# Kernel optimization log

Measured on AMD Instinct MI355X. Metric: run time of the kernel, lower is better.

Reference implementation:

```python
import jax, jax.numpy as jnp
import numpy as np

D_MODEL = 1024
N_HEADS = 16
D_HEAD = D_MODEL // N_HEADS
EPS = 1e-5


def setup_inputs() -> dict:
    key = jax.random.key(0)
    ks = jax.random.split(key, 7)
    B, T = 4, 2048
    s = 1.0 / np.sqrt(D_MODEL)
    return {
        "x": jax.random.normal(ks[0], (B, T, D_MODEL), dtype=jnp.float32),
        "ln_g": jnp.ones((D_MODEL,), jnp.float32),
        "ln_b": jnp.zeros((D_MODEL,), jnp.float32),
        "W_qkv": jax.random.normal(ks[1], (D_MODEL, 3 * D_MODEL), jnp.float32) * s,
        "b_qkv": jnp.zeros((3 * D_MODEL,), jnp.float32),
        "W_gate": jax.random.normal(ks[2], (D_MODEL, D_MODEL), jnp.float32) * s,
        "b_gate": jnp.zeros((D_MODEL,), jnp.float32),
        "W_proj": jax.random.normal(ks[3], (D_MODEL, D_MODEL), jnp.float32) * s,
        "b_proj": jnp.zeros((D_MODEL,), jnp.float32),
    }


def _forward(x, ln_g, ln_b, W_qkv, b_qkv, W_gate, b_gate, W_proj, b_proj):
    B, T, D = x.shape
    H, d = N_HEADS, D_HEAD
    # LayerNorm (eps=1e-5, biased variance as in torch)
    mu = jnp.mean(x, axis=-1, keepdims=True)
    var = jnp.mean((x - mu) ** 2, axis=-1, keepdims=True)
    x_norm = (x - mu) * jax.lax.rsqrt(var + EPS) * ln_g + ln_b
    qkv = x_norm @ W_qkv + b_qkv
    q, k, v = jnp.split(qkv, 3, axis=-1)  # each [B,T,D]
    # concept gate uses raw x
    gate = jax.nn.sigmoid(x @ W_gate + b_gate)
    gate = gate / (jnp.mean(gate, axis=-1, keepdims=True) + EPS)
    q = (q * gate).reshape(B, T, H, d)
    k = (k * gate).reshape(B, T, H, d)
    v = v.reshape(B, T, H, d)
    # ReLU^2 feature map in fp32
    q = jax.nn.relu(q.astype(jnp.float32)) ** 2 + EPS
    k = jax.nn.relu(k.astype(jnp.float32)) ** 2 + EPS
    v = v.astype(jnp.float32)
    # causal linear attention via kv recurrence (scan over T, T-major)
    qT = jnp.transpose(q, (1, 0, 2, 3))  # [T,B,H,d]
    kT = jnp.transpose(k, (1, 0, 2, 3))
    vT = jnp.transpose(v, (1, 0, 2, 3))

    def step(carry, inp):
        kv_s, k_s = carry  # [B,H,d,d], [B,H,d]
        q_t, k_t, v_t = inp  # [B,H,d]
        kv_s = kv_s + k_t[..., :, None] * v_t[..., None, :]
        k_s = k_s + k_t
        num = jnp.einsum('bhd,bhdm->bhm', q_t, kv_s)
        den = jnp.einsum('bhd,bhd->bh', q_t, k_s)[..., None] + EPS
        return (kv_s, k_s), num / den

    init = (jnp.zeros((B, H, d, d), jnp.float32), jnp.zeros((B, H, d), jnp.float32))
    _, outT = jax.lax.scan(step, init, (qT, kT, vT))  # [T,B,H,d]
    out = jnp.transpose(outT, (1, 0, 2, 3)).astype(x.dtype).reshape(B, T, D)
    return out @ W_proj + b_proj


def reference(x, ln_g, ln_b, W_qkv, b_qkv, W_gate, b_gate, W_proj, b_proj):
    return _forward(x, ln_g, ln_b, W_qkv, b_qkv, W_gate, b_gate, W_proj, b_proj)
```

## Files before the change

kernel.cpp:

```cpp
#include <hip/hip_runtime.h>
#include <math.h>

#define TOK 8192
#define DM 1024
#define EPSF 1e-5f

typedef __attribute__((ext_vector_type(8))) short short8;
typedef __attribute__((ext_vector_type(4))) float f32x4;

static __device__ __forceinline__ ushort f2bf(float f) {
  unsigned u = __float_as_uint(f);
  unsigned r = (u + 0x7fffu + ((u >> 16) & 1u)) >> 16;
  return (ushort)r;
}
static __device__ __forceinline__ float bf2f(ushort u) {
  return __uint_as_float((unsigned)u << 16);
}

static __device__ __forceinline__ void gload_lds16(const ushort* g, ushort* l) {
  __builtin_amdgcn_global_load_lds((const __attribute__((address_space(1))) void*)g,
                                   (__attribute__((address_space(3))) void*)l, 16, 0, 0);
}

static __device__ __forceinline__ int cswz(int row) {
  return (((row & 7) ^ ((row >> 3) & 7)) << 3);
}

__global__ __launch_bounds__(256) void prep_k(
    const float* __restrict__ x, const float* __restrict__ g,
    const float* __restrict__ b, ushort* __restrict__ x_b,
    ushort* __restrict__ xn_b,
    const float* __restrict__ Wg, const float* __restrict__ Wq,
    const float* __restrict__ Wp, ushort* __restrict__ Wtg,
    ushort* __restrict__ Wtq, ushort* __restrict__ Wtp) {
  __shared__ ushort tile[32][33];
  __shared__ float red[8];
  if (blockIdx.x < 8192) {
    int row = blockIdx.x;
    const float4* xr = (const float4*)(x + (size_t)row * DM);
    float4 v = xr[threadIdx.x];
    ushort4 xb4;
    xb4.x = f2bf(v.x); xb4.y = f2bf(v.y); xb4.z = f2bf(v.z); xb4.w = f2bf(v.w);
    ((ushort4*)(x_b + (size_t)row * DM))[threadIdx.x] = xb4;
    float s = v.x + v.y + v.z + v.w;
#pragma unroll
    for (int o = 32; o > 0; o >>= 1) s += __shfl_down(s, o, 64);
    int lane = threadIdx.x & 63, w = threadIdx.x >> 6;
    if (lane == 0) red[w] = s;
    __syncthreads();
    float mu = (red[0] + red[1] + red[2] + red[3]) * (1.0f / DM);
    float dx = v.x - mu, dy = v.y - mu, dz = v.z - mu, dw = v.w - mu;
    float ss = dx * dx + dy * dy + dz * dz + dw * dw;
#pragma unroll
    for (int o = 32; o > 0; o >>= 1) ss += __shfl_down(ss, o, 64);
    if (lane == 0) red[4 + w] = ss;
    __syncthreads();
    float var = (red[4] + red[5] + red[6] + red[7]) * (1.0f / DM);
    float rstd = rsqrtf(var + EPSF);
    float4 gg = ((const float4*)g)[threadIdx.x];
    float4 bb = ((const float4*)b)[threadIdx.x];
    ushort4 o4;
    o4.x = f2bf(dx * rstd * gg.x + bb.x);
    o4.y = f2bf(dy * rstd * gg.y + bb.y);
    o4.z = f2bf(dz * rstd * gg.z + bb.z);
    o4.w = f2bf(dw * rstd * gg.w + bb.w);
    ((ushort4*)(xn_b + (size_t)row * DM))[threadIdx.x] = o4;
  } else {
    int bid = blockIdx.x - 8192;
    const float* W; ushort* Wt; int N; int local;
    if (bid < 1024)      { W = Wg; Wt = Wtg; N = 1024; local = bid; }
    else if (bid < 4096) { W = Wq; Wt = Wtq; N = 3072; local = bid - 1024; }
    else                 { W = Wp; Wt = Wtp; N = 1024; local = bid - 4096; }
    int ntiles = N >> 5;
    int n0 = (local % ntiles) * 32, k0 = (local / ntiles) * 32;
    int tx = threadIdx.x & 31, ty = threadIdx.x >> 5;
#pragma unroll
    for (int i = 0; i < 4; i++) {
      int k = ty + i * 8;
      tile[k][tx] = f2bf(W[(size_t)(k0 + k) * N + n0 + tx]);
    }
    __syncthreads();
#pragma unroll
    for (int i = 0; i < 4; i++) {
      int n = ty + i * 8;
      Wt[(size_t)(n0 + n) * 1024 + k0 + tx] = tile[tx][n];
    }
  }
}

#define BM 128
#define BN 128
#define BK 64

static __device__ __forceinline__ void stage_tile128(
    const ushort* __restrict__ A, const ushort* __restrict__ Bt,
    int m0, int n0, int k0, int K, ushort* As, ushort* Bs, int w, int lane) {
#pragma unroll
  for (int j = 0; j < 4; j++) {
    int lu = (w * 4 + j) * 64 + lane;
    int r = lu >> 3;
    int kb = (lu & 7) ^ (r & 7);
    gload_lds16(A + (size_t)(m0 + r) * K + k0 + kb * 8, As + (w * 4 + j) * 512);
    gload_lds16(Bt + (size_t)(n0 + r) * K + k0 + kb * 8, Bs + (w * 4 + j) * 512);
  }
}

static __device__ __forceinline__ void compute_tile128(
    const ushort* as, const ushort* bs, int wr, int wc, int lane, f32x4 acc[4][4]) {
#pragma unroll
  for (int ks = 0; ks < 2; ks++) {
    short8 af[4], bfr[4];
    int kq = ks * 4 + (lane >> 4);
#pragma unroll
    for (int f = 0; f < 4; f++) {
      int ra = wr * 64 + f * 16 + (lane & 15);
      af[f] = *(const short8*)&as[(ra * 8 + (kq ^ (ra & 7))) * 8];
      int rb = wc * 64 + f * 16 + (lane & 15);
      bfr[f] = *(const short8*)&bs[(rb * 8 + (kq ^ (rb & 7))) * 8];
    }
#pragma unroll
    for (int i = 0; i < 4; i++)
#pragma unroll
      for (int j2 = 0; j2 < 4; j2++)
        acc[i][j2] = __builtin_amdgcn_mfma_f32_16x16x32_bf16(af[i], bfr[j2], acc[i][j2], 0, 0, 0);
  }
}

#define GEMM_LOOP128(A_, B_, m0_, n0_, K_)                                       \
  f32x4 acc[4][4] = {};                                                          \
  stage_tile128(A_, B_, m0_, n0_, 0, K_, sh, sh + 16384, w, lane);               \
  int nt = (K_) / BK;                                                            \
  for (int t = 0; t < nt; t++) {                                                 \
    __syncthreads();                                                             \
    if (t + 1 < nt)                                                              \
      stage_tile128(A_, B_, m0_, n0_, (t + 1) * BK, K_,                          \
                    sh + ((t + 1) & 1) * 8192, sh + 16384 + ((t + 1) & 1) * 8192,\
                    w, lane);                                                    \
    compute_tile128(sh + (t & 1) * 8192, sh + 16384 + (t & 1) * 8192,            \
                    wr, wc, lane, acc);                                          \
  }                                                                              \
  __syncthreads();

__global__ __launch_bounds__(256) void gemm_bf16_k(
    const ushort* __restrict__ A, const ushort* __restrict__ Bt,
    const float* __restrict__ bias, float* __restrict__ Cf, int ldc, int K) {
  __shared__ __align__(16) ushort sh[32768];
  int tid = threadIdx.x, lane = tid & 63, w = tid >> 6;
  int m0 = blockIdx.y * BM, n0 = blockIdx.x * BN;
  int wr = w >> 1, wc = w & 1;
  GEMM_LOOP128(A, Bt, m0, n0, K)
#pragma unroll
  for (int i = 0; i < 4; i++) {
#pragma unroll
    for (int j2 = 0; j2 < 4; j2++) {
      int col = n0 + wc * 64 + j2 * 16 + (lane & 15);
      float bv = bias[col];
#pragma unroll
      for (int r = 0; r < 4; r++) {
        int row = m0 + wr * 64 + i * 16 + (lane >> 4) * 4 + r;
        Cf[(size_t)row * ldc + col] = acc[i][j2][r] + bv;
      }
    }
  }
}

__global__ __launch_bounds__(256) void gemm_gate_k(
    const ushort* __restrict__ A, const ushort* __restrict__ Bt,
    const float* __restrict__ bias, ushort* __restrict__ Cb, int ldc, int K,
    float* __restrict__ gpart) {
  __shared__ __align__(16) ushort sh[32768];
  int tid = threadIdx.x, lane = tid & 63, w = tid >> 6;
  int m0 = blockIdx.y * BM, n0 = blockIdx.x * BN;
  int wr = w >> 1, wc = w & 1;
  GEMM_LOOP128(A, Bt, m0, n0, K)
  int lr = lane & 15, lg = lane >> 4;
  float* rs2 = (float*)sh;
#pragma unroll
  for (int i = 0; i < 4; i++) {
#pragma unroll
    for (int r = 0; r < 4; r++) {
      float rsum = 0.0f;
      int row = m0 + wr * 64 + i * 16 + lg * 4 + r;
#pragma unroll
      for (int j2 = 0; j2 < 4; j2++) {
        int col = n0 + wc * 64 + j2 * 16 + lr;
        float v = 1.0f / (1.0f + __expf(-(acc[i][j2][r] + bias[col])));
        rsum += v;
        Cb[(size_t)row * ldc + col] = f2bf(v);
      }
#pragma unroll
      for (int o = 1; o < 16; o <<= 1) rsum += __shfl_xor(rsum, o, 64);
      if (lr == 0) rs2[wc * 128 + wr * 64 + i * 16 + lg * 4 + r] = rsum;
    }
  }
  __syncthreads();
  if (tid < 128)
    gpart[(size_t)(m0 + tid) * 8 + blockIdx.x] = rs2[tid] + rs2[128 + tid];
}

__global__ __launch_bounds__(256) void gemm_qkv_k(
    const ushort* __restrict__ A, const ushort* __restrict__ Bt,
    const float* __restrict__ bias, const ushort* __restrict__ gate_b,
    const float* __restrict__ gpart,
    ushort* __restrict__ qb, ushort* __restrict__ kb,
    ushort* __restrict__ kt, ushort* __restrict__ vt, int K) {
  __shared__ __align__(16) ushort sh[32768];
  __shared__ float ginvs[128];
  int tid = threadIdx.x, lane = tid & 63, w = tid >> 6;
  int m0 = blockIdx.y * BM, n0 = blockIdx.x * BN;
  int wr = w >> 1, wc = w & 1;
  GEMM_LOOP128(A, Bt, m0, n0, K)
  int region = n0 >> 10;
  int n0b = n0 & 1023;
  int h0 = n0b >> 6;
  if (region < 2) {
    if (tid < 128) {
      const float4* gp = (const float4*)&gpart[(size_t)(m0 + tid) * 8];
      float4 s0 = gp[0], s1 = gp[1];
      float s = s0.x + s0.y + s0.z + s0.w + s1.x + s1.y + s1.z + s1.w;
      ginvs[tid] = 1.0f / (s * (1.0f / DM) + EPSF);
    }
#pragma unroll
    for (int it = 0; it < 8; it++) {
      int e = it * 256 + tid;
      int row = e >> 4, ch = e & 15;
      *(short8*)&sh[row * 132 + ch * 8] =
          *(const short8*)&gate_b[(size_t)(m0 + row) * DM + n0b + ch * 8];
    }
    __syncthreads();
#pragma unroll
    for (int i = 0; i < 4; i++) {
#pragma unroll
      for (int j2 = 0; j2 < 4; j2++) {
        int cl = wc * 64 + j2 * 16 + (lane & 15);
        float bv = bias[n0 + cl];
        int rl0 = wr * 64 + i * 16 + (lane >> 4) * 4;
#pragma unroll
        for (int r = 0; r < 4; r++) {
          float gv = bf2f(sh[(rl0 + r) * 132 + cl]) * ginvs[rl0 + r];
          float v = (acc[i][j2][r] + bv) * gv;
          v = fmaxf(v, 0.0f);
          acc[i][j2][r] = v * v + EPSF;
        }
      }
    }
    __syncthreads();
  } else {
#pragma unroll
    for (int i = 0; i < 4; i++)
#pragma unroll
      for (int j2 = 0; j2 < 4; j2++) {
        int cl = wc * 64 + j2 * 16 + (lane & 15);
        float bv = bias[n0 + cl];
#pragma unroll
        for (int r = 0; r < 4; r++) acc[i][j2][r] += bv;
      }
  }
#pragma unroll
  for (int i = 0; i < 4; i++) {
#pragma unroll
    for (int j2 = 0; j2 < 4; j2++) {
      int cl = wc * 64 + j2 * 16 + (lane & 15);
      int rl0 = wr * 64 + i * 16 + (lane >> 4) * 4;
#pragma unroll
      for (int r = 0; r < 4; r++) {
        int row = rl0 + r;
        sh[row * 128 + (cl ^ cswz(row))] = f2bf(acc[i][j2][r]);
      }
    }
  }
  __syncthreads();
  if (region < 2) {
    ushort* dstRM = (region == 0) ? qb : kb;
#pragma unroll
    for (int it = 0; it < 8; it++) {
      int e = it * 256 + tid;
      int row = e >> 4, ch = e & 15;
      short8 val = *(const short8*)&sh[row * 128 + ((ch * 8) ^ cswz(row))];
      int tglob = m0 + row;
      size_t bh2 = (size_t)(tglob >> 11) * 16 + h0 + (ch >> 3);
      *(short8*)&dstRM[(bh2 * 2048 + (tglob & 2047)) * 64 + (ch & 7) * 8] = val;
    }
  }
  if (region >= 1) {
    ushort* dstT = (region == 1) ? kt : vt;
#pragma unroll
    for (int it = 0; it < 8; it++) {
      int e = it * 256 + tid;
      int tch = e & 15, dkrow = e >> 4;
      short8 val;
#pragma unroll
      for (int j = 0; j < 8; j++) {
        int row = tch * 8 + j;
        val[j] = (short)sh[row * 128 + (dkrow ^ cswz(row))];
      }
      int tglob0 = m0 + tch * 8;
      size_t bh2 = (size_t)(tglob0 >> 11) * 16 + h0 + (dkrow >> 6);
      *(short8*)&dstT[(bh2 * 64 + (dkrow & 63)) * 2048 + (tglob0 & 2047)] = val;
    }
  }
}

__global__ __launch_bounds__(256) void chunkpfx_k(const ushort* __restrict__ kt,
                                                  const ushort* __restrict__ vt,
                                                  ushort* __restrict__ KVb,
                                                  float* __restrict__ ksum) {
  int bid = blockIdx.x;
  int bh = (bid & 7) | ((bid >> 5) << 3);
  int dvs = (bid >> 3) & 3;
  int tid = threadIdx.x, l = tid & 63, w = tid >> 6;
  int lg = l >> 4;
  const ushort* vT = vt + ((size_t)bh * 64 + dvs * 16 + (l & 15)) * 2048;
  const ushort* kT = kt + ((size_t)bh * 64 + w * 16 + (l & 15)) * 2048;
  f32x4 run = {0.f, 0.f, 0.f, 0.f};
  float runks = 0.0f;
  short8 a0 = *(const short8*)&vT[lg * 8];
  short8 a1 = *(const short8*)&vT[32 + lg * 8];
  short8 b0 = *(const short8*)&kT[lg * 8];
  short8 b1 = *(const short8*)&kT[32 + lg * 8];
  for (int c = 0; c < 32; c++) {
    ushort* dst = KVb + ((size_t)bh * 32 + c) * 4096 +
                  (size_t)(dvs * 16 + lg * 4) * 64 + w * 16 + (l & 15);
    dst[0] = f2bf(run[0]); dst[64] = f2bf(run[1]);
    dst[128] = f2bf(run[2]); dst[192] = f2bf(run[3]);
    if (dvs == 0) {
      float s = 0.f;
#pragma unroll
      for (int j = 0; j < 8; j++) s += bf2f((ushort)b0[j]) + bf2f((ushort)b1[j]);
      s += __shfl_xor(s, 16, 64);
      s += __shfl_xor(s, 32, 64);
      if (l < 16) ksum[((size_t)bh * 32 + c) * 64 + w * 16 + l] = runks;
      runks += s;
    }
    int cn = (c + 1) & 31;
    short8 na0 = *(const short8*)&vT[cn * 64 + lg * 8];
    short8 na1 = *(const short8*)&vT[cn * 64 + 32 + lg * 8];
    short8 nb0 = *(const short8*)&kT[cn * 64 + lg * 8];
    short8 nb1 = *(const short8*)&kT[cn * 64 + 32 + lg * 8];
    run = __builtin_amdgcn_mfma_f32_16x16x32_bf16(a0, b0, run, 0, 0, 0);
    run = __builtin_amdgcn_mfma_f32_16x16x32_bf16(a1, b1, run, 0, 0, 0);
    a0 = na0; a1 = na1; b0 = nb0; b1 = nb1;
  }
}

__global__ __launch_bounds__(256) void attn_k(
    const ushort* __restrict__ qb, const ushort* __restrict__ kb,
    const ushort* __restrict__ vt, const ushort* __restrict__ KVb,
    const float* __restrict__ ks, ushort* __restrict__ attnout) {
  int c = blockIdx.x, bh = blockIdx.y;
  int b = bh >> 4, h = bh & 15;
  const ushort* qB = qb + ((size_t)bh * 2048 + (size_t)c * 64) * 64;
  const ushort* kB = kb + ((size_t)bh * 2048 + (size_t)c * 64) * 64;
  const ushort* vT = vt + (size_t)bh * 64 * 2048 + (size_t)c * 64;
  const ushort* kvB = KVb + ((size_t)bh * 32 + c) * 4096;
  const float* ksP = ks + ((size_t)bh * 32 + c) * 64;
  __shared__ __align__(16) char SL[64 * 128];
  __shared__ float denp[4][64];
  __shared__ float den2p[4][64];
  __shared__ float invden[64];
  int tid = threadIdx.x, l = tid & 63, w = tid >> 6;
  int lr = l & 15, lg = l >> 4;
  {
    short8 q0 = *(const short8*)&qB[(size_t)l * 64 + w * 16];
    short8 q1 = *(const short8*)&qB[(size_t)l * 64 + w * 16 + 8];
    float d2 = 0.0f;
#pragma unroll
    for (int j = 0; j < 8; j++) {
      d2 += bf2f((ushort)q0[j]) * ksP[w * 16 + j];
      d2 += bf2f((ushort)q1[j]) * ksP[w * 16 + 8 + j];
    }
    den2p[w][l] = d2;
  }
#pragma unroll
  for (int n = 0; n < 4; n++) {
    f32x4 sa = {0.f, 0.f, 0.f, 0.f};
#pragma unroll
    for (int g = 0; g < 2; g++) {
      short8 a = *(const short8*)&kB[(size_t)(w * 16 + lr) * 64 + g * 32 + lg * 8];
      short8 bq = *(const short8*)&qB[(size_t)(n * 16 + lr) * 64 + g * 32 + lg * 8];
      sa = __builtin_amdgcn_mfma_f32_16x16x32_bf16(a, bq, sa, 0, 0, 0);
    }
    int t = n * 16 + lr;
    int s0 = w * 16 + lg * 4;
    float dsum = 0.0f;
    ushort sb[4];
#pragma unroll
    for (int r = 0; r < 4; r++) {
      float v = (s0 + r <= t) ? sa[r] : 0.0f;
      dsum += v;
      sb[r] = f2bf(v);
    }
    dsum += __shfl_xor(dsum, 16, 64);
    dsum += __shfl_xor(dsum, 32, 64);
    if (l < 16) denp[w][n * 16 + l] = dsum;
    int u = (s0 >> 3) ^ (t & 7);
    uint2 p;
    p.x = sb[0] | ((unsigned)sb[1] << 16);
    p.y = sb[2] | ((unsigned)sb[3] << 16);
    *(uint2*)&SL[t * 128 + u * 16 + (s0 & 7) * 2] = p;
  }
  __syncthreads();
  if (tid < 64) {
    float den = denp[0][tid] + denp[1][tid] + denp[2][tid] + denp[3][tid] +
                den2p[0][tid] + den2p[1][tid] + den2p[2][tid] + den2p[3][tid] + EPSF;
    invden[tid] = 1.0f / den;
  }
  __syncthreads();
#pragma unroll
  for (int n = 0; n < 4; n++) {
    f32x4 oa = {0.f, 0.f, 0.f, 0.f};
#pragma unroll
    for (int g = 0; g < 2; g++) {
      short8 a = *(const short8*)&kvB[(size_t)(w * 16 + lr) * 64 + g * 32 + lg * 8];
      short8 bq = *(const short8*)&qB[(size_t)(n * 16 + lr) * 64 + g * 32 + lg * 8];
      oa = __builtin_amdgcn_mfma_f32_16x16x32_bf16(a, bq, oa, 0, 0, 0);
    }
    int t = n * 16 + lr;
#pragma unroll
    for (int g = 0; g < 2; g++) {
      short8 a = *(const short8*)&vT[(size_t)(w * 16 + lr) * 2048 + g * 32 + lg * 8];
      int u = (g * 4 + lg) ^ (t & 7);
      short8 bs = *(const short8*)&SL[t * 128 + u * 16];
      oa = __builtin_amdgcn_mfma_f32_16x16x32_bf16(a, bs, oa, 0, 0, 0);
    }
    float iv = invden[t];
    ushort ob[4];
#pragma unroll
    for (int r = 0; r < 4; r++) ob[r] = f2bf(oa[r] * iv);
    size_t tok = (size_t)b * 2048 + (size_t)c * 64 + t;
    uint2 p;
    p.x = ob[0] | ((unsigned)ob[1] << 16);
    p.y = ob[2] | ((unsigned)ob[3] << 16);
    *(uint2*)&attnout[tok * 1024 + h * 64 + w * 16 + lg * 4] = p;
  }
}

extern "C" void kernel_launch(void* const* d_in, const int* in_sizes, int n_in,
                              void* d_out, int out_size, void* d_ws, size_t ws_size,
                              hipStream_t stream) {
  const float* x      = (const float*)d_in[0];
  const float* ln_g   = (const float*)d_in[1];
  const float* ln_b   = (const float*)d_in[2];
  const float* W_qkv  = (const float*)d_in[3];
  const float* b_qkv  = (const float*)d_in[4];
  const float* W_gate = (const float*)d_in[5];
  const float* b_gate = (const float*)d_in[6];
  const float* W_proj = (const float*)d_in[7];
  const float* b_proj = (const float*)d_in[8];
  float* out = (float*)d_out;

  char* wsb = (char*)d_ws;
  const size_t TD = (size_t)TOK * DM;
  const size_t SLOT = TD * 2;
  ushort* x_b     = (ushort*)(wsb + 0 * SLOT);
  ushort* attnout = (ushort*)(wsb + 0 * SLOT);
  ushort* xn_b    = (ushort*)(wsb + 1 * SLOT);
  ushort* qb      = (ushort*)(wsb + 2 * SLOT);
  ushort* kb      = (ushort*)(wsb + 3 * SLOT);
  ushort* kt      = (ushort*)(wsb + 4 * SLOT);
  ushort* vt      = (ushort*)(wsb + 5 * SLOT);
  ushort* gate_b  = (ushort*)(wsb + 6 * SLOT);
  ushort* Wt_qkv  = (ushort*)(wsb + 8 * SLOT);
  ushort* Wt_gate = (ushort*)(wsb + 8 * SLOT + (size_t)8 * 1024 * 1024);
  ushort* KVb     = (ushort*)(wsb + 8 * SLOT);
  ushort* Wt_proj = (ushort*)(wsb + 9 * SLOT);
  float*  ksum    = (float*)(wsb + 9 * SLOT + (size_t)8 * 1024 * 1024);
  float*  gpart   = (float*)(wsb + 9 * SLOT + (size_t)12 * 1024 * 1024);

  prep_k<<<8192 + 5120, 256, 0, stream>>>(x, ln_g, ln_b, x_b, xn_b,
                                          W_gate, W_qkv, W_proj,
                                          Wt_gate, Wt_qkv, Wt_proj);
  gemm_gate_k<<<dim3(DM / BN, TOK / BM), 256, 0, stream>>>(x_b, Wt_gate, b_gate,
                                                           gate_b, DM, DM, gpart);
  gemm_qkv_k<<<dim3(3 * DM / BN, TOK / BM), 256, 0, stream>>>(xn_b, Wt_qkv, b_qkv, gate_b,
                                                              gpart, qb, kb, kt, vt, DM);
  chunkpfx_k<<<256, 256, 0, stream>>>(kt, vt, KVb, ksum);
  attn_k<<<dim3(32, 64), 256, 0, stream>>>(qb, kb, vt, KVb, ksum, attnout);
  gemm_bf16_k<<<dim3(DM / BN, TOK / BM), 256, 0, stream>>>(attnout, Wt_proj, b_proj, out,
                                                           DM, DM);
}
```

Baseline: 187.0 us.

## Fuse chunk prefix-state kernel into attention kernel with sequential chunk loop

Merges the chunk KV prefix-sum kernel and the per-chunk attention kernel into one kernel. Each block owns a (batch-head, 16-wide dv slice) and walks all 32 chunks in order, keeping the running KV state in registers and staging it through LDS instead of writing KVb and ksum to global memory. This removes a kernel launch and the global round trip for the chunk states. In exchange it drops from 2048 parallel blocks to 256 serial-over-chunks blocks, and the intra-chunk QK^T scores and denominator are recomputed by each of the four dv-slice blocks.

```diff
diff --git a/kernel.cpp b/kernel.cpp
--- a/kernel.cpp
+++ b/kernel.cpp
@@ -301,128 +301,110 @@
   }
 }
 
-__global__ __launch_bounds__(256) void chunkpfx_k(const ushort* __restrict__ kt,
-                                                  const ushort* __restrict__ vt,
-                                                  ushort* __restrict__ KVb,
-                                                  float* __restrict__ ksum) {
+__global__ __launch_bounds__(256) void attn_fused_k(
+    const ushort* __restrict__ qb, const ushort* __restrict__ kb,
+    const ushort* __restrict__ vt, const ushort* __restrict__ kt,
+    ushort* __restrict__ attnout) {
   int bid = blockIdx.x;
   int bh = (bid & 7) | ((bid >> 5) << 3);
   int dvs = (bid >> 3) & 3;
-  int tid = threadIdx.x, l = tid & 63, w = tid >> 6;
-  int lg = l >> 4;
-  const ushort* vT = vt + ((size_t)bh * 64 + dvs * 16 + (l & 15)) * 2048;
-  const ushort* kT = kt + ((size_t)bh * 64 + w * 16 + (l & 15)) * 2048;
-  f32x4 run = {0.f, 0.f, 0.f, 0.f};
-  float runks = 0.0f;
-  short8 a0 = *(const short8*)&vT[lg * 8];
-  short8 a1 = *(const short8*)&vT[32 + lg * 8];
-  short8 b0 = *(const short8*)&kT[lg * 8];
-  short8 b1 = *(const short8*)&kT[32 + lg * 8];
-  for (int c = 0; c < 32; c++) {
-    ushort* dst = KVb + ((size_t)bh * 32 + c) * 4096 +
-                  (size_t)(dvs * 16 + lg * 4) * 64 + w * 16 + (l & 15);
-    dst[0] = f2bf(run[0]); dst[64] = f2bf(run[1]);
-    dst[128] = f2bf(run[2]); dst[192] = f2bf(run[3]);
-    if (dvs == 0) {
-      float s = 0.f;
-#pragma unroll
-      for (int j = 0; j < 8; j++) s += bf2f((ushort)b0[j]) + bf2f((ushort)b1[j]);
-      s += __shfl_xor(s, 16, 64);
-      s += __shfl_xor(s, 32, 64);
-      if (l < 16) ksum[((size_t)bh * 32 + c) * 64 + w * 16 + l] = runks;
-      runks += s;
-    }
-    int cn = (c + 1) & 31;
-    short8 na0 = *(const short8*)&vT[cn * 64 + lg * 8];
-    short8 na1 = *(const short8*)&vT[cn * 64 + 32 + lg * 8];
-    short8 nb0 = *(const short8*)&kT[cn * 64 + lg * 8];
-    short8 nb1 = *(const short8*)&kT[cn * 64 + 32 + lg * 8];
-    run = __builtin_amdgcn_mfma_f32_16x16x32_bf16(a0, b0, run, 0, 0, 0);
-    run = __builtin_amdgcn_mfma_f32_16x16x32_bf16(a1, b1, run, 0, 0, 0);
-    a0 = na0; a1 = na1; b0 = nb0; b1 = nb1;
-  }
-}
-
-__global__ __launch_bounds__(256) void attn_k(
-    const ushort* __restrict__ qb, const ushort* __restrict__ kb,
-    const ushort* __restrict__ vt, const ushort* __restrict__ KVb,
-    const float* __restrict__ ks, ushort* __restrict__ attnout) {
-  int c = blockIdx.x, bh = blockIdx.y;
   int b = bh >> 4, h = bh & 15;
-  const ushort* qB = qb + ((size_t)bh * 2048 + (size_t)c * 64) * 64;
-  const ushort* kB = kb + ((size_t)bh * 2048 + (size_t)c * 64) * 64;
-  const ushort* vT = vt + (size_t)bh * 64 * 2048 + (size_t)c * 64;
-  const ushort* kvB = KVb + ((size_t)bh * 32 + c) * 4096;
-  const float* ksP = ks + ((size_t)bh * 32 + c) * 64;
+  const ushort* qB0 = qb + (size_t)bh * 2048 * 64;
+  const ushort* kB0 = kb + (size_t)bh * 2048 * 64;
+  const ushort* vT = vt + ((size_t)bh * 64 + dvs * 16) * 2048;
+  const ushort* kT = kt + (size_t)bh * 64 * 2048;
   __shared__ __align__(16) char SL[64 * 128];
+  __shared__ __align__(16) ushort KVL[16 * 64];
+  __shared__ float ksL[64];
   __shared__ float denp[4][64];
-  __shared__ float den2p[4][64];
   __shared__ float invden[64];
   int tid = threadIdx.x, l = tid & 63, w = tid >> 6;
   int lr = l & 15, lg = l >> 4;
-  {
-    short8 q0 = *(const short8*)&qB[(size_t)l * 64 + w * 16];
-    short8 q1 = *(const short8*)&qB[(size_t)l * 64 + w * 16 + 8];
-    float d2 = 0.0f;
-#pragma unroll
-    for (int j = 0; j < 8; j++) {
-      d2 += bf2f((ushort)q0[j]) * ksP[w * 16 + j];
-      d2 += bf2f((ushort)q1[j]) * ksP[w * 16 + 8 + j];
-    }
-    den2p[w][l] = d2;
-  }
-#pragma unroll
-  for (int n = 0; n < 4; n++) {
-    f32x4 sa = {0.f, 0.f, 0.f, 0.f};
+  f32x4 kvrun = {0.f, 0.f, 0.f, 0.f};
+  float runks = 0.0f;
+  for (int c = 0; c < 32; c++) {
+    const ushort* qB = qB0 + (size_t)c * 64 * 64;
+    const ushort* kB = kB0 + (size_t)c * 64 * 64;
+    short8 ka[2], ktf[2], vtf[2], bq[4][2];
 #pragma unroll
     for (int g = 0; g < 2; g++) {
-      short8 a = *(const short8*)&kB[(size_t)(w * 16 + lr) * 64 + g * 32 + lg * 8];
-      short8 bq = *(const short8*)&qB[(size_t)(n * 16 + lr) * 64 + g * 32 + lg * 8];
-      sa = __builtin_amdgcn_mfma_f32_16x16x32_bf16(a, bq, sa, 0, 0, 0);
-    }
-    int t = n * 16 + lr;
-    int s0 = w * 16 + lg * 4;
-    float dsum = 0.0f;
-    ushort sb[4];
+      ka[g]  = *(const short8*)&kB[(size_t)(w * 16 + lr) * 64 + g * 32 + lg * 8];
+      ktf[g] = *(const short8*)&kT[(size_t)(w * 16 + lr) * 2048 + c * 64 + g * 32 + lg * 8];
+      vtf[g] = *(const short8*)&vT[(size_t)lr * 2048 + c * 64 + g * 32 + lg * 8];
+#pragma unroll
+      for (int n = 0; n < 4; n++)
+        bq[n][g] = *(const short8*)&qB[(size_t)(n * 16 + lr) * 64 + g * 32 + lg * 8];
+    }
+#pragma unroll
+    for (int n = 0; n < 4; n++) {
+      f32x4 sa = {0.f, 0.f, 0.f, 0.f};
+      sa = __builtin_amdgcn_mfma_f32_16x16x32_bf16(ka[0], bq[n][0], sa, 0, 0, 0);
+      sa = __builtin_amdgcn_mfma_f32_16x16x32_bf16(ka[1], bq[n][1], sa, 0, 0, 0);
+      int t = n * 16 + lr;
+      int s0 = w * 16 + lg * 4;
+      float dsum = 0.0f;
+      ushort sb[4];
+#pragma unroll
+      for (int r = 0; r < 4; r++) {
+        float v = (s0 + r <= t) ? sa[r] : 0.0f;
+        dsum += v;
+        sb[r] = f2bf(v);
+      }
+      dsum += __shfl_xor(dsum, 16, 64);
+      dsum += __shfl_xor(dsum, 32, 64);
+      if (l < 16) denp[w][n * 16 + l] = dsum;
+      int u = (s0 >> 3) ^ (t & 7);
+      uint2 p;
+      p.x = sb[0] | ((unsigned)sb[1] << 16);
+      p.y = sb[2] | ((unsigned)sb[3] << 16);
+      *(uint2*)&SL[t * 128 + u * 16 + (s0 & 7) * 2] = p;
+    }
 #pragma unroll
     for (int r = 0; r < 4; r++) {
-      float v = (s0 + r <= t) ? sa[r] : 0.0f;
-      dsum += v;
-      sb[r] = f2bf(v);
-    }
-    dsum += __shfl_xor(dsum, 16, 64);
-    dsum += __shfl_xor(dsum, 32, 64);
-    if (l < 16) denp[w][n * 16 + l] = dsum;
-    int u = (s0 >> 3) ^ (t & 7);
-    uint2 p;
-    p.x = sb[0] | ((unsigned)sb[1] << 16);
-    p.y = sb[2] | ((unsigned)sb[3] << 16);
-    *(uint2*)&SL[t * 128 + u * 16 + (s0 & 7) * 2] = p;
-  }
-  __syncthreads();
-  if (tid < 64) {
-    float den = denp[0][tid] + denp[1][tid] + denp[2][tid] + denp[3][tid] +
-                den2p[0][tid] + den2p[1][tid] + den2p[2][tid] + den2p[3][tid] + EPSF;
-    invden[tid] = 1.0f / den;
-  }
-  __syncthreads();
-#pragma unroll
-  for (int n = 0; n < 4; n++) {
+      int dv = lg * 4 + r, dk = w * 16 + lr;
+      KVL[dv * 64 + (((dk >> 3) ^ (dv & 7)) << 3) + (dk & 7)] = f2bf(kvrun[r]);
+    }
+    {
+      float s = 0.f;
+#pragma unroll
+      for (int j = 0; j < 8; j++) s += bf2f((ushort)ktf[0][j]) + bf2f((ushort)ktf[1][j]);
+      s += __shfl_xor(s, 16, 64);
+      s += __shfl_xor(s, 32, 64);
+      if (l < 16) ksL[w * 16 + lr] = runks;
+      runks += s;
+    }
+    kvrun = __builtin_amdgcn_mfma_f32_16x16x32_bf16(vtf[0], ktf[0], kvrun, 0, 0, 0);
+    kvrun = __builtin_amdgcn_mfma_f32_16x16x32_bf16(vtf[1], ktf[1], kvrun, 0, 0, 0);
+    __syncthreads();
     f32x4 oa = {0.f, 0.f, 0.f, 0.f};
+    int t = w * 16 + lr;
 #pragma unroll
     for (int g = 0; g < 2; g++) {
-      short8 a = *(const short8*)&kvB[(size_t)(w * 16 + lr) * 64 + g * 32 + lg * 8];
-      short8 bq = *(const short8*)&qB[(size_t)(n * 16 + lr) * 64 + g * 32 + lg * 8];
-      oa = __builtin_amdgcn_mfma_f32_16x16x32_bf16(a, bq, oa, 0, 0, 0);
-    }
-    int t = n * 16 + lr;
-#pragma unroll
-    for (int g = 0; g < 2; g++) {
-      short8 a = *(const short8*)&vT[(size_t)(w * 16 + lr) * 2048 + g * 32 + lg * 8];
-      int u = (g * 4 + lg) ^ (t & 7);
-      short8 bs = *(const short8*)&SL[t * 128 + u * 16];
-      oa = __builtin_amdgcn_mfma_f32_16x16x32_bf16(a, bs, oa, 0, 0, 0);
-    }
+      short8 kvlf = *(const short8*)&KVL[lr * 64 + ((((g << 2) + lg) ^ (lr & 7)) << 3)];
+      oa = __builtin_amdgcn_mfma_f32_16x16x32_bf16(kvlf, bq[w][g], oa, 0, 0, 0);
+      int u = ((g << 2) + lg) ^ (t & 7);
+      short8 slf = *(const short8*)&SL[t * 128 + u * 16];
+      oa = __builtin_amdgcn_mfma_f32_16x16x32_bf16(vtf[g], slf, oa, 0, 0, 0);
+    }
+    if (w == 0) {
+#pragma unroll
+      for (int n = 0; n < 4; n++) {
+        float d2 = 0.f;
+#pragma unroll
+        for (int g = 0; g < 2; g++)
+#pragma unroll
+          for (int j = 0; j < 8; j++)
+            d2 += bf2f((ushort)bq[n][g][j]) * ksL[g * 32 + lg * 8 + j];
+        d2 += __shfl_xor(d2, 16, 64);
+        d2 += __shfl_xor(d2, 32, 64);
+        if (l < 16) {
+          int tt = n * 16 + l;
+          invden[tt] = 1.0f / (denp[0][tt] + denp[1][tt] + denp[2][tt] + denp[3][tt] +
+                               d2 + EPSF);
+        }
+      }
+    }
+    __syncthreads();
     float iv = invden[t];
     ushort ob[4];
 #pragma unroll
@@ -431,7 +413,7 @@
     uint2 p;
     p.x = ob[0] | ((unsigned)ob[1] << 16);
     p.y = ob[2] | ((unsigned)ob[3] << 16);
-    *(uint2*)&attnout[tok * 1024 + h * 64 + w * 16 + lg * 4] = p;
+    *(uint2*)&attnout[tok * 1024 + h * 64 + dvs * 16 + lg * 4] = p;
   }
 }
 
@@ -462,9 +444,7 @@
   ushort* gate_b  = (ushort*)(wsb + 6 * SLOT);
   ushort* Wt_qkv  = (ushort*)(wsb + 8 * SLOT);
   ushort* Wt_gate = (ushort*)(wsb + 8 * SLOT + (size_t)8 * 1024 * 1024);
-  ushort* KVb     = (ushort*)(wsb + 8 * SLOT);
   ushort* Wt_proj = (ushort*)(wsb + 9 * SLOT);
-  float*  ksum    = (float*)(wsb + 9 * SLOT + (size_t)8 * 1024 * 1024);
   float*  gpart   = (float*)(wsb + 9 * SLOT + (size_t)12 * 1024 * 1024);
 
   prep_k<<<8192 + 5120, 256, 0, stream>>>(x, ln_g, ln_b, x_b, xn_b,
@@ -474,8 +454,7 @@
                                                            gate_b, DM, DM, gpart);
   gemm_qkv_k<<<dim3(3 * DM / BN, TOK / BM), 256, 0, stream>>>(xn_b, Wt_qkv, b_qkv, gate_b,
                                                               gpart, qb, kb, kt, vt, DM);
-  chunkpfx_k<<<256, 256, 0, stream>>>(kt, vt, KVb, ksum);
-  attn_k<<<dim3(32, 64), 256, 0, stream>>>(qb, kb, vt, KVb, ksum, attnout);
+  attn_fused_k<<<256, 256, 0, stream>>>(qb, kb, vt, kt, attnout);
   gemm_bf16_k<<<dim3(DM / BN, TOK / BM), 256, 0, stream>>>(attnout, Wt_proj, b_proj, out,
                                                            DM, DM);
 }
```

After: 463.2 us. +147.7%, slower.
